# Performance work log

Measured on AMD Instinct MI355X. Metric: run time of the kernel, lower is better.

The kernel has to match this reference:

```python
import jax, jax.numpy as jnp
import numpy as np

B, S, D = 2, 2048, 1024
H, DH = 16, 64
WINDOW = 256


def setup_inputs() -> dict:
    key = jax.random.key(0)
    ks = jax.random.split(key, 11)
    s = 1.0 / np.sqrt(D)
    return {
        "query": jax.random.normal(ks[0], (B, S, D), jnp.float32),
        "key": jax.random.normal(ks[1], (B, S, D), jnp.float32),
        "value": jax.random.normal(ks[2], (B, S, D), jnp.float32),
        "Wq": jax.random.normal(ks[3], (D, D), jnp.float32) * s,
        "bq": jax.random.normal(ks[4], (D,), jnp.float32) * s,
        "Wk": jax.random.normal(ks[5], (D, D), jnp.float32) * s,
        "bk": jax.random.normal(ks[6], (D,), jnp.float32) * s,
        "Wv": jax.random.normal(ks[7], (D, D), jnp.float32) * s,
        "bv": jax.random.normal(ks[8], (D,), jnp.float32) * s,
        "Wo": jax.random.normal(ks[9], (D, D), jnp.float32) * s,
        "bo": jax.random.normal(ks[10], (D,), jnp.float32) * s,
    }


def reference(query, key, value, Wq, bq, Wk, bk, Wv, bv, Wo, bo):
    scale = DH ** -0.5
    # projections (torch Linear: x @ W.T + b)
    q = query @ Wq.T + bq  # [B,S,D]
    k = key @ Wk.T + bk
    v = value @ Wv.T + bv
    # split heads -> [B,H,S,DH]
    q = q.reshape(B, S, H, DH).transpose(0, 2, 1, 3)
    k = k.reshape(B, S, H, DH).transpose(0, 2, 1, 3)
    v = v.reshape(B, S, H, DH).transpose(0, 2, 1, 3)
    # dense scores with sliding-window causal mask
    attn = jnp.einsum('bhqd,bhkd->bhqk', q, k) * scale  # [B,H,S,S]
    q_idx = jnp.arange(S)[:, None]
    k_idx = jnp.arange(S)[None, :]
    keep = (k_idx <= q_idx) & (k_idx >= q_idx - WINDOW + 1)  # causal & window
    attn = jnp.where(keep[None, None], attn, -jnp.inf)
    attn = jax.nn.softmax(attn, axis=-1)
    # dropout_p=0.0 (eval) -> identity
    out = jnp.einsum('bhqk,bhkd->bhqd', attn, v)  # [B,H,S,DH]
    out = out.transpose(0, 2, 1, 3).reshape(B, S, D)
    return out @ Wo.T + bo
```

## Files before the change

kernel.cpp:

```cpp
#include <hip/hip_runtime.h>
#include <cstdint>
#include <cstddef>

#define B_   2
#define S_   2048
#define D_   1024
#define H_   16
#define DH_  64
#define NROW (B_ * S_)

typedef __bf16  bf16x8 __attribute__((ext_vector_type(8)));
typedef __bf16  bf16x4 __attribute__((ext_vector_type(4)));
typedef float   f32x4  __attribute__((ext_vector_type(4)));

#define MFMA16(a, b, c) __builtin_amdgcn_mfma_f32_16x16x32_bf16((a), (b), (c), 0, 0, 0)

__device__ __forceinline__ void gload_lds16(const void* g, void* l) {
  __builtin_amdgcn_global_load_lds(
      (__attribute__((address_space(1))) void*)(g),
      (__attribute__((address_space(3))) void*)(l), 16, 0, 0);
}

struct CastArgs { const float* src[7]; __bf16* dst[7]; };

__global__ void cast_all(CastArgs a) {
  int b = blockIdx.x, which, idx;
  if (b < 12288) { which = b >> 12; idx = b & 4095; }
  else { b -= 12288; which = 3 + (b >> 10); idx = b & 1023; }
  const int i = idx * 256 + threadIdx.x;
  const float4 v = ((const float4*)a.src[which])[i];
  bf16x4 o;
  o[0] = (__bf16)v.x; o[1] = (__bf16)v.y; o[2] = (__bf16)v.z; o[3] = (__bf16)v.w;
  ((bf16x4*)a.dst[which])[i] = o;
}

struct QKVArgs {
  const __bf16* A[3]; const __bf16* W[3]; const float* bias[3]; __bf16* C[3];
};

__global__ __launch_bounds__(256, 2) void gemm_qkv(QKVArgs args) {
  __shared__ __bf16 As[128 * 32];
  __shared__ __bf16 Bs[128 * 32];
  const int z = blockIdx.z;
  const __bf16* A = args.A[z];
  const __bf16* W = args.W[z];
  const float* bias = args.bias[z];
  __bf16* C = args.C[z];
  const int tid  = threadIdx.x;
  const int lane = tid & 63, wave = tid >> 6;
  const int lo   = lane & 15, quad = lane >> 4;
  const int wr   = wave & 1,  wc   = wave >> 1;
  const int bn   = blockIdx.x, bm = blockIdx.y;
  const __bf16* Ag = A + (size_t)bn * 128 * D_;
  const __bf16* Wg = W + (size_t)bm * 128 * D_;
  const int c0 = tid, c1 = tid + 256;
  const int r0 = c0 >> 2, s0 = (c0 & 3) * 8;
  const int r1 = c1 >> 2, s1 = (c1 & 3) * 8;

  f32x4 acc[4][4] = {};
  for (int k0 = 0; k0 < D_; k0 += 32) {
    __syncthreads();
    gload_lds16(Ag + (size_t)r0 * D_ + k0 + s0, &As[c0 * 8]);
    gload_lds16(Ag + (size_t)r1 * D_ + k0 + s1, &As[c1 * 8]);
    gload_lds16(Wg + (size_t)r0 * D_ + k0 + s0, &Bs[c0 * 8]);
    gload_lds16(Wg + (size_t)r1 * D_ + k0 + s1, &Bs[c1 * 8]);
    __syncthreads();
    bf16x8 af[4], bfr[4];
#pragma unroll
    for (int i = 0; i < 4; i++)
      af[i] = *(const bf16x8*)&As[(wr * 64 + i * 16 + lo) * 32 + quad * 8];
#pragma unroll
    for (int j = 0; j < 4; j++)
      bfr[j] = *(const bf16x8*)&Bs[(wc * 64 + j * 16 + lo) * 32 + quad * 8];
#pragma unroll
    for (int i = 0; i < 4; i++)
#pragma unroll
      for (int j = 0; j < 4; j++)
        acc[i][j] = MFMA16(af[i], bfr[j], acc[i][j]);
  }
  if (z == 2) {
#pragma unroll
    for (int i = 0; i < 4; i++) {
      const int row0 = bn * 128 + wr * 64 + i * 16 + quad * 4;
      const int bb = row0 >> 11, s = row0 & (S_ - 1);
#pragma unroll
      for (int j = 0; j < 4; j++) {
        const int col = bm * 128 + wc * 64 + j * 16 + lo;
        const int hh = col >> 6, dd = col & 63;
        const float bv = bias[col];
        bf16x4 o;
#pragma unroll
        for (int r = 0; r < 4; r++) o[r] = (__bf16)(acc[i][j][r] + bv);
        *(bf16x4*)&C[((size_t)(bb * H_ + hh) * DH_ + dd) * S_ + s] = o;
      }
    }
  } else {
#pragma unroll
    for (int i = 0; i < 4; i++) {
      const int row = bn * 128 + wr * 64 + i * 16 + quad * 4;
#pragma unroll
      for (int j = 0; j < 4; j++) {
        const int col = bm * 128 + wc * 64 + j * 16 + lo;
        const float bv = bias[col];
#pragma unroll
        for (int r = 0; r < 4; r++)
          C[(size_t)(row + r) * D_ + col] = (__bf16)(acc[i][j][r] + bv);
      }
    }
  }
}

__global__ __launch_bounds__(256, 3) void attn_win5(
    const __bf16* __restrict__ Qp, const __bf16* __restrict__ Kp,
    const __bf16* __restrict__ Vt, __bf16* __restrict__ ctx) {
  __shared__ __bf16 smem[25600];
  const int qt = blockIdx.x, h = blockIdx.y, b = blockIdx.z;
  const int q0 = qt * 128;
  const int tid = threadIdx.x, wave = tid >> 6, lane = tid & 63;
  const int lo = lane & 15, quad = lane >> 4;
  const int tmin = (q0 >= 256) ? 0 : ((256 - q0) >> 6);
  const __bf16* Kg = Kp + (size_t)b * S_ * D_ + h * DH_;
  const __bf16* Vg = Vt + (size_t)(b * H_ + h) * DH_ * S_;
  const size_t qbase = ((size_t)b * S_) * D_ + h * DH_;

  const int c0 = tid, c1 = tid + 256;
  const int rA = c0 >> 3, gA = ((c0 & 7) ^ (rA & 7)) * 8;
  const int rB = c1 >> 3, gB = ((c1 & 7) ^ (rB & 7)) * 8;

  auto stageK = [&](int t) {
    const int k0 = q0 - 256 + t * 64;
    const int kb = (t & 1) * 4096;
    gload_lds16(Kg + (size_t)(k0 + rA) * D_ + gA, &smem[kb + c0 * 8]);
    gload_lds16(Kg + (size_t)(k0 + rB) * D_ + gB, &smem[kb + c1 * 8]);
  };
  auto stageV = [&](int t) {
    const int k0 = q0 - 256 + t * 64;
    const int vb = 8192 + (t & 1) * 4096;
    gload_lds16(Vg + (size_t)rA * S_ + k0 + gA, &smem[vb + c0 * 8]);
    gload_lds16(Vg + (size_t)rB * S_ + k0 + gB, &smem[vb + c1 * 8]);
  };

  bf16x8 qf[2][2];
#pragma unroll
  for (int f = 0; f < 2; f++) {
    const int qr = q0 + wave * 32 + f * 16 + lo;
    qf[f][0] = *(const bf16x8*)&Qp[qbase + (size_t)qr * D_ + quad * 8];
    qf[f][1] = *(const bf16x8*)&Qp[qbase + (size_t)qr * D_ + 32 + quad * 8];
  }

  stageK(tmin); stageV(tmin);
  stageK(tmin + 1); stageV(tmin + 1);
  __syncthreads();

  const int g0 = (quad ^ (lo & 7)) * 8;
  const int g1 = ((quad + 4) ^ (lo & 7)) * 8;

  const int pwb = 16384 + wave * 2304;
  float rs[2][4] = {};
  f32x4 oacc[2][4] = {};

#pragma unroll
  for (int t = 0; t < 6; t++) {
    if (t < tmin) continue;
    const int kb = (t & 1) * 4096, vb = 8192 + (t & 1) * 4096;
    const int kmin = t * 64 - 256;
    const bool active =
        (kmin <= wave * 32 + 31) && (kmin + 63 > wave * 32 - 256);
    if (active) {
      f32x4 sc[2][4];
#pragma unroll
      for (int kt = 0; kt < 4; kt++) {
        const int kr = kt * 16 + lo;
        const bf16x8 kf0 = *(const bf16x8*)&smem[kb + kr * 64 + g0];
        const bf16x8 kf1 = *(const bf16x8*)&smem[kb + kr * 64 + g1];
#pragma unroll
        for (int f = 0; f < 2; f++) {
          f32x4 c = {0.f, 0.f, 0.f, 0.f};
          c = MFMA16(qf[f][0], kf0, c);
          c = MFMA16(qf[f][1], kf1, c);
          sc[f][kt] = c;
        }
      }
#pragma unroll
      for (int f = 0; f < 2; f++)
#pragma unroll
        for (int kt = 0; kt < 4; kt++)
#pragma unroll
          for (int r = 0; r < 4; r++) {
            const int delta =
                kmin + kt * 16 + lo - (wave * 32 + f * 16 + quad * 4 + r);
            const bool keep = (delta <= 0) && (delta > -256);
            const float e = __expf(fmaf(sc[f][kt][r], 0.125f, -8.0f));
            const float p = keep ? e : 0.0f;
            sc[f][kt][r] = p;
            rs[f][r] += p;
          }
#pragma unroll
      for (int f = 0; f < 2; f++)
#pragma unroll
        for (int kt = 0; kt < 4; kt++)
#pragma unroll
          for (int r = 0; r < 4; r++)
            smem[pwb + (f * 16 + quad * 4 + r) * 72 + kt * 16 + lo] =
                (__bf16)sc[f][kt][r];
      bf16x8 pf[2][2];
#pragma unroll
      for (int f = 0; f < 2; f++) {
        pf[f][0] = *(const bf16x8*)&smem[pwb + (f * 16 + lo) * 72 + quad * 8];
        pf[f][1] = *(const bf16x8*)&smem[pwb + (f * 16 + lo) * 72 + 32 + quad * 8];
      }
#pragma unroll
      for (int ds = 0; ds < 4; ds++) {
        const bf16x8 vf0 = *(const bf16x8*)&smem[vb + (ds * 16 + lo) * 64 + g0];
        const bf16x8 vf1 = *(const bf16x8*)&smem[vb + (ds * 16 + lo) * 64 + g1];
#pragma unroll
        for (int f = 0; f < 2; f++) {
          oacc[f][ds] = MFMA16(pf[f][0], vf0, oacc[f][ds]);
          oacc[f][ds] = MFMA16(pf[f][1], vf1, oacc[f][ds]);
        }
      }
    }
    if (t < 5) {
      __syncthreads();
      if (t + 2 <= 5) { stageK(t + 2); stageV(t + 2); }
    }
  }

#pragma unroll
  for (int f = 0; f < 2; f++)
#pragma unroll
    for (int r = 0; r < 4; r++)
#pragma unroll
      for (int off = 1; off < 16; off <<= 1)
        rs[f][r] += __shfl_xor(rs[f][r], off);

#pragma unroll
  for (int f = 0; f < 2; f++)
#pragma unroll
    for (int ds = 0; ds < 4; ds++)
#pragma unroll
      for (int r = 0; r < 4; r++) {
        const int qg = q0 + wave * 32 + f * 16 + quad * 4 + r;
        ctx[((size_t)b * S_ + qg) * D_ + h * DH_ + ds * 16 + lo] =
            (__bf16)(oacc[f][ds][r] / rs[f][r]);
      }
}

__global__ __launch_bounds__(256, 2) void gemm_o(
    const __bf16* __restrict__ A, const __bf16* __restrict__ W,
    const float* __restrict__ bias, float* __restrict__ C) {
  __shared__ __bf16 As[64 * 32];
  __shared__ __bf16 Bs[128 * 32];
  const int tid = threadIdx.x, lane = tid & 63, wave = tid >> 6;
  const int lo = lane & 15, quad = lane >> 4;
  const int wr = wave & 1, wc = wave >> 1;
  const int bn = blockIdx.x, bm = blockIdx.y;
  const __bf16* Ag = A + (size_t)bn * 64 * D_;
  const __bf16* Wg = W + (size_t)bm * 128 * D_;
  const int ra = tid >> 2, sa = (tid & 3) * 8;
  const int cb0 = tid, cb1 = tid + 256;
  const int rb0 = cb0 >> 2, sb0 = (cb0 & 3) * 8;
  const int rb1 = cb1 >> 2, sb1 = (cb1 & 3) * 8;
  f32x4 acc[2][4] = {};
  for (int k0 = 0; k0 < D_; k0 += 32) {
    __syncthreads();
    gload_lds16(Ag + (size_t)ra * D_ + k0 + sa, &As[tid * 8]);
    gload_lds16(Wg + (size_t)rb0 * D_ + k0 + sb0, &Bs[cb0 * 8]);
    gload_lds16(Wg + (size_t)rb1 * D_ + k0 + sb1, &Bs[cb1 * 8]);
    __syncthreads();
    bf16x8 af[2], bfr[4];
#pragma unroll
    for (int i = 0; i < 2; i++)
      af[i] = *(const bf16x8*)&As[(wr * 32 + i * 16 + lo) * 32 + quad * 8];
#pragma unroll
    for (int j = 0; j < 4; j++)
      bfr[j] = *(const bf16x8*)&Bs[(wc * 64 + j * 16 + lo) * 32 + quad * 8];
#pragma unroll
    for (int i = 0; i < 2; i++)
#pragma unroll
      for (int j = 0; j < 4; j++)
        acc[i][j] = MFMA16(af[i], bfr[j], acc[i][j]);
  }
#pragma unroll
  for (int i = 0; i < 2; i++) {
    const int row = bn * 64 + wr * 32 + i * 16 + quad * 4;
#pragma unroll
    for (int j = 0; j < 4; j++) {
      const int col = bm * 128 + wc * 64 + j * 16 + lo;
      const float bv = bias[col];
#pragma unroll
      for (int r = 0; r < 4; r++)
        C[(size_t)(row + r) * D_ + col] = acc[i][j][r] + bv;
    }
  }
}

extern "C" void kernel_launch(void* const* d_in, const int* in_sizes, int n_in,
                              void* d_out, int out_size, void* d_ws, size_t ws_size,
                              hipStream_t stream) {
  (void)in_sizes; (void)n_in; (void)out_size; (void)ws_size;
  const float* q_in = (const float*)d_in[0];
  const float* k_in = (const float*)d_in[1];
  const float* v_in = (const float*)d_in[2];
  const float* Wq   = (const float*)d_in[3];
  const float* bq   = (const float*)d_in[4];
  const float* Wk   = (const float*)d_in[5];
  const float* bk   = (const float*)d_in[6];
  const float* Wv   = (const float*)d_in[7];
  const float* bv   = (const float*)d_in[8];
  const float* Wo   = (const float*)d_in[9];
  const float* bo   = (const float*)d_in[10];

  const size_t XN = (size_t)NROW * D_;
  const size_t WN = (size_t)D_ * D_;
  char* ws = (char*)d_ws;
  __bf16* xq  = (__bf16*)ws; ws += XN * 2;
  __bf16* xk  = (__bf16*)ws; ws += XN * 2;
  __bf16* xv  = (__bf16*)ws; ws += XN * 2;
  __bf16* wqb = (__bf16*)ws; ws += WN * 2;
  __bf16* wkb = (__bf16*)ws; ws += WN * 2;
  __bf16* wvb = (__bf16*)ws; ws += WN * 2;
  __bf16* wob = (__bf16*)ws; ws += WN * 2;
  __bf16* Qp  = (__bf16*)ws; ws += XN * 2;
  __bf16* Kp  = (__bf16*)ws; ws += XN * 2;
  __bf16* Vtp = (__bf16*)ws; ws += XN * 2;
  __bf16* ctx = (__bf16*)ws; ws += XN * 2;

  CastArgs ca;
  ca.src[0] = q_in; ca.src[1] = k_in; ca.src[2] = v_in;
  ca.src[3] = Wq; ca.src[4] = Wk; ca.src[5] = Wv; ca.src[6] = Wo;
  ca.dst[0] = xq; ca.dst[1] = xk; ca.dst[2] = xv;
  ca.dst[3] = wqb; ca.dst[4] = wkb; ca.dst[5] = wvb; ca.dst[6] = wob;
  cast_all<<<16384, 256, 0, stream>>>(ca);

  QKVArgs qa;
  qa.A[0] = xq;  qa.A[1] = xk;  qa.A[2] = xv;
  qa.W[0] = wqb; qa.W[1] = wkb; qa.W[2] = wvb;
  qa.bias[0] = bq; qa.bias[1] = bk; qa.bias[2] = bv;
  qa.C[0] = Qp; qa.C[1] = Kp; qa.C[2] = Vtp;
  gemm_qkv<<<dim3(NROW / 128, D_ / 128, 3), 256, 0, stream>>>(qa);

  attn_win5<<<dim3(S_ / 128, H_, B_), 256, 0, stream>>>(Qp, Kp, Vtp, ctx);

  gemm_o<<<dim3(NROW / 64, D_ / 128), 256, 0, stream>>>(ctx, wob, bo, (float*)d_out);
}
```

Baseline: 194.9 us.

## Fuse activation fp32-to-bf16 cast into QKV GEMM and swizzle LDS tiles

The QKV projection GEMM now loads fp32 activations directly into shared memory and converts them to bf16 in registers. This removes the separate activation cast pass and its bf16 intermediate buffers; only the weights are cast beforehand. XOR swizzling is added to the LDS tile layouts of both the QKV and output GEMMs to reduce bank conflicts. The cost is doubled shared-memory footprint and global traffic for the A tiles, plus conversion instructions inside the GEMM inner loop.

```diff
diff --git a/kernel.cpp b/kernel.cpp
--- a/kernel.cpp
+++ b/kernel.cpp
@@ -21,13 +21,11 @@
       (__attribute__((address_space(3))) void*)(l), 16, 0, 0);
 }
 
-struct CastArgs { const float* src[7]; __bf16* dst[7]; };
-
-__global__ void cast_all(CastArgs a) {
-  int b = blockIdx.x, which, idx;
-  if (b < 12288) { which = b >> 12; idx = b & 4095; }
-  else { b -= 12288; which = 3 + (b >> 10); idx = b & 1023; }
-  const int i = idx * 256 + threadIdx.x;
+struct CastWArgs { const float* src[4]; __bf16* dst[4]; };
+
+__global__ void cast_w(CastWArgs a) {
+  const int which = blockIdx.y;
+  const int i = blockIdx.x * blockDim.x + threadIdx.x;
   const float4 v = ((const float4*)a.src[which])[i];
   bf16x4 o;
   o[0] = (__bf16)v.x; o[1] = (__bf16)v.y; o[2] = (__bf16)v.z; o[3] = (__bf16)v.w;
@@ -35,14 +33,14 @@
 }
 
 struct QKVArgs {
-  const __bf16* A[3]; const __bf16* W[3]; const float* bias[3]; __bf16* C[3];
+  const float* A[3]; const __bf16* W[3]; const float* bias[3]; __bf16* C[3];
 };
 
 __global__ __launch_bounds__(256, 2) void gemm_qkv(QKVArgs args) {
-  __shared__ __bf16 As[128 * 32];
+  __shared__ float  Asf[128 * 32];
   __shared__ __bf16 Bs[128 * 32];
   const int z = blockIdx.z;
-  const __bf16* A = args.A[z];
+  const float* A = args.A[z];
   const __bf16* W = args.W[z];
   const float* bias = args.bias[z];
   __bf16* C = args.C[z];
@@ -51,27 +49,40 @@
   const int lo   = lane & 15, quad = lane >> 4;
   const int wr   = wave & 1,  wc   = wave >> 1;
   const int bn   = blockIdx.x, bm = blockIdx.y;
-  const __bf16* Ag = A + (size_t)bn * 128 * D_;
+  const float*  Ag = A + (size_t)bn * 128 * D_;
   const __bf16* Wg = W + (size_t)bm * 128 * D_;
-  const int c0 = tid, c1 = tid + 256;
-  const int r0 = c0 >> 2, s0 = (c0 & 3) * 8;
-  const int r1 = c1 >> 2, s1 = (c1 & 3) * 8;
+  const int ar0 = tid >> 3,          as0 = ((tid & 7) ^ (ar0 & 7)) * 4;
+  const int ar1 = (tid + 256) >> 3,  as1 = (((tid + 256) & 7) ^ (ar1 & 7)) * 4;
+  const int ar2 = (tid + 512) >> 3,  as2 = (((tid + 512) & 7) ^ (ar2 & 7)) * 4;
+  const int ar3 = (tid + 768) >> 3,  as3 = (((tid + 768) & 7) ^ (ar3 & 7)) * 4;
+  const int br0 = tid >> 2,          bs0 = (((tid) & 3) ^ (br0 & 3)) * 8;
+  const int br1 = (tid + 256) >> 2,  bs1 = (((tid + 256) & 3) ^ (br1 & 3)) * 8;
 
   f32x4 acc[4][4] = {};
   for (int k0 = 0; k0 < D_; k0 += 32) {
     __syncthreads();
-    gload_lds16(Ag + (size_t)r0 * D_ + k0 + s0, &As[c0 * 8]);
-    gload_lds16(Ag + (size_t)r1 * D_ + k0 + s1, &As[c1 * 8]);
-    gload_lds16(Wg + (size_t)r0 * D_ + k0 + s0, &Bs[c0 * 8]);
-    gload_lds16(Wg + (size_t)r1 * D_ + k0 + s1, &Bs[c1 * 8]);
+    gload_lds16(Ag + (size_t)ar0 * D_ + k0 + as0, &Asf[tid * 4]);
+    gload_lds16(Ag + (size_t)ar1 * D_ + k0 + as1, &Asf[(tid + 256) * 4]);
+    gload_lds16(Ag + (size_t)ar2 * D_ + k0 + as2, &Asf[(tid + 512) * 4]);
+    gload_lds16(Ag + (size_t)ar3 * D_ + k0 + as3, &Asf[(tid + 768) * 4]);
+    gload_lds16(Wg + (size_t)br0 * D_ + k0 + bs0, &Bs[tid * 8]);
+    gload_lds16(Wg + (size_t)br1 * D_ + k0 + bs1, &Bs[(tid + 256) * 8]);
     __syncthreads();
     bf16x8 af[4], bfr[4];
-#pragma unroll
-    for (int i = 0; i < 4; i++)
-      af[i] = *(const bf16x8*)&As[(wr * 64 + i * 16 + lo) * 32 + quad * 8];
+    const int m7 = lo & 7, m3 = lo & 3;
+#pragma unroll
+    for (int i = 0; i < 4; i++) {
+      const int row = wr * 64 + i * 16 + lo;
+      const f32x4 a0 = *(const f32x4*)&Asf[row * 32 + ((2 * quad) ^ m7) * 4];
+      const f32x4 a1 = *(const f32x4*)&Asf[row * 32 + ((2 * quad + 1) ^ m7) * 4];
+      bf16x8 v;
+#pragma unroll
+      for (int j = 0; j < 4; j++) { v[j] = (__bf16)a0[j]; v[4 + j] = (__bf16)a1[j]; }
+      af[i] = v;
+    }
 #pragma unroll
     for (int j = 0; j < 4; j++)
-      bfr[j] = *(const bf16x8*)&Bs[(wc * 64 + j * 16 + lo) * 32 + quad * 8];
+      bfr[j] = *(const bf16x8*)&Bs[(wc * 64 + j * 16 + lo) * 32 + (quad ^ m3) * 8];
 #pragma unroll
     for (int i = 0; i < 4; i++)
 #pragma unroll
@@ -257,24 +268,24 @@
   const int bn = blockIdx.x, bm = blockIdx.y;
   const __bf16* Ag = A + (size_t)bn * 64 * D_;
   const __bf16* Wg = W + (size_t)bm * 128 * D_;
-  const int ra = tid >> 2, sa = (tid & 3) * 8;
-  const int cb0 = tid, cb1 = tid + 256;
-  const int rb0 = cb0 >> 2, sb0 = (cb0 & 3) * 8;
-  const int rb1 = cb1 >> 2, sb1 = (cb1 & 3) * 8;
+  const int ra = tid >> 2,          sa = (((tid) & 3) ^ (ra & 3)) * 8;
+  const int rb0 = tid >> 2,         sb0 = (((tid) & 3) ^ (rb0 & 3)) * 8;
+  const int rb1 = (tid + 256) >> 2, sb1 = (((tid + 256) & 3) ^ (rb1 & 3)) * 8;
   f32x4 acc[2][4] = {};
   for (int k0 = 0; k0 < D_; k0 += 32) {
     __syncthreads();
     gload_lds16(Ag + (size_t)ra * D_ + k0 + sa, &As[tid * 8]);
-    gload_lds16(Wg + (size_t)rb0 * D_ + k0 + sb0, &Bs[cb0 * 8]);
-    gload_lds16(Wg + (size_t)rb1 * D_ + k0 + sb1, &Bs[cb1 * 8]);
+    gload_lds16(Wg + (size_t)rb0 * D_ + k0 + sb0, &Bs[tid * 8]);
+    gload_lds16(Wg + (size_t)rb1 * D_ + k0 + sb1, &Bs[(tid + 256) * 8]);
     __syncthreads();
     bf16x8 af[2], bfr[4];
+    const int m3 = lo & 3;
 #pragma unroll
     for (int i = 0; i < 2; i++)
-      af[i] = *(const bf16x8*)&As[(wr * 32 + i * 16 + lo) * 32 + quad * 8];
+      af[i] = *(const bf16x8*)&As[(wr * 32 + i * 16 + lo) * 32 + (quad ^ m3) * 8];
 #pragma unroll
     for (int j = 0; j < 4; j++)
-      bfr[j] = *(const bf16x8*)&Bs[(wc * 64 + j * 16 + lo) * 32 + quad * 8];
+      bfr[j] = *(const bf16x8*)&Bs[(wc * 64 + j * 16 + lo) * 32 + (quad ^ m3) * 8];
 #pragma unroll
     for (int i = 0; i < 2; i++)
 #pragma unroll
@@ -314,9 +325,6 @@
   const size_t XN = (size_t)NROW * D_;
   const size_t WN = (size_t)D_ * D_;
   char* ws = (char*)d_ws;
-  __bf16* xq  = (__bf16*)ws; ws += XN * 2;
-  __bf16* xk  = (__bf16*)ws; ws += XN * 2;
-  __bf16* xv  = (__bf16*)ws; ws += XN * 2;
   __bf16* wqb = (__bf16*)ws; ws += WN * 2;
   __bf16* wkb = (__bf16*)ws; ws += WN * 2;
   __bf16* wvb = (__bf16*)ws; ws += WN * 2;
@@ -326,16 +334,14 @@
   __bf16* Vtp = (__bf16*)ws; ws += XN * 2;
   __bf16* ctx = (__bf16*)ws; ws += XN * 2;
 
-  CastArgs ca;
-  ca.src[0] = q_in; ca.src[1] = k_in; ca.src[2] = v_in;
-  ca.src[3] = Wq; ca.src[4] = Wk; ca.src[5] = Wv; ca.src[6] = Wo;
-  ca.dst[0] = xq; ca.dst[1] = xk; ca.dst[2] = xv;
-  ca.dst[3] = wqb; ca.dst[4] = wkb; ca.dst[5] = wvb; ca.dst[6] = wob;
-  cast_all<<<16384, 256, 0, stream>>>(ca);
+  CastWArgs cw;
+  cw.src[0] = Wq; cw.src[1] = Wk; cw.src[2] = Wv; cw.src[3] = Wo;
+  cw.dst[0] = wqb; cw.dst[1] = wkb; cw.dst[2] = wvb; cw.dst[3] = wob;
+  cast_w<<<dim3((int)(WN / 4 / 256), 4), 256, 0, stream>>>(cw);
 
   QKVArgs qa;
-  qa.A[0] = xq;  qa.A[1] = xk;  qa.A[2] = xv;
-  qa.W[0] = wqb; qa.W[1] = wkb; qa.W[2] = wvb;
+  qa.A[0] = q_in; qa.A[1] = k_in; qa.A[2] = v_in;
+  qa.W[0] = wqb;  qa.W[1] = wkb;  qa.W[2] = wvb;
   qa.bias[0] = bq; qa.bias[1] = bk; qa.bias[2] = bv;
   qa.C[0] = Qp; qa.C[1] = Kp; qa.C[2] = Vtp;
   gemm_qkv<<<dim3(NROW / 128, D_ / 128, 3), 256, 0, stream>>>(qa);
```

After: 209.6 us. 7.6% more time.
